# Performance work log

Measured on AMD Instinct MI355X. Metric: run time of the kernel, lower is better.

## Reference

```python
import jax, jax.numpy as jnp
import numpy as np

S, B, N, DIM = 64, 4, 256, 256
HEADS, DIM_HEAD = 8, 32
INNER = HEADS * DIM_HEAD  # 256
SCALE = DIM_HEAD ** -0.5
NEG = -1e10


def setup_inputs() -> dict:
    key = jax.random.key(0)
    k1, k2, k3, k4, k5 = jax.random.split(key, 5)
    x = jax.random.normal(k1, (S, B, N, DIM), dtype=jnp.float32)
    mask = jax.random.randint(k2, (S, N, N), 0, 2, dtype=jnp.int32)
    # nn.Linear(dim, inner*3, bias=False): y = x @ W_qkv  (W stored transposed)
    W_qkv = jax.random.normal(k3, (DIM, 3 * INNER), dtype=jnp.float32) / np.sqrt(DIM)
    W_out = jax.random.normal(k4, (INNER, DIM), dtype=jnp.float32) / np.sqrt(INNER)
    b_out = jax.random.normal(k5, (DIM,), dtype=jnp.float32) * 0.01
    return {"x": x, "mask": mask, "W_qkv": W_qkv, "W_out": W_out, "b_out": b_out}


def reference(x, mask, W_qkv, W_out, b_out):
    s, b, n, _ = x.shape
    qkv = x @ W_qkv                                  # [s,b,n,3*inner]
    q, k, v = jnp.split(qkv, 3, axis=-1)
    def to_heads(t):
        # s b n (h d) -> s b h n d
        return t.reshape(s, b, n, HEADS, DIM_HEAD).transpose(0, 1, 3, 2, 4)
    q, k, v = to_heads(q), to_heads(k), to_heads(v)
    sim = jnp.einsum('sbhid,sbhjd->sbhij', q, k) * SCALE
    sim = jnp.where(mask[:, None, None, :, :] == 0, NEG, sim)
    attn = jax.nn.softmax(sim, axis=-1)
    out = jnp.einsum('sbhij,sbhjd->sbhid', attn, v)
    out = out.transpose(0, 1, 3, 2, 4).reshape(s, b, n, INNER)  # s b h n d -> s b n (h d)
    return out @ W_out + b_out
```

## Files before the change

kernel.cpp:

```cpp
#include <hip/hip_runtime.h>

typedef __attribute__((ext_vector_type(8))) short bf16x8;
typedef __attribute__((ext_vector_type(4))) float f32x4;

__device__ __forceinline__ unsigned short f2bf(float f) {
  unsigned int u = __builtin_bit_cast(unsigned int, f);
  u += 0x7fffu + ((u >> 16) & 1u);
  return (unsigned short)(u >> 16);
}

__device__ __forceinline__ unsigned int cvt_pk_bf16(float lo, float hi) {
  unsigned int r;
  asm("v_cvt_pk_bf16_f32 %0, %1, %2" : "=v"(r) : "v"(lo), "v"(hi));
  return r;
}

typedef const __attribute__((address_space(1))) unsigned int* as1_u32p;
typedef __attribute__((address_space(3))) unsigned int* as3_u32p;
__device__ __forceinline__ void glds16(const void* g, void* l) {
  __builtin_amdgcn_global_load_lds((as1_u32p)g, (as3_u32p)l, 16, 0, 0);
}

__global__ __launch_bounds__(256) void cvt_kernel(const float* __restrict__ X,
                                                  unsigned short* __restrict__ Y) {
  const long long i = ((long long)blockIdx.x * 256 + threadIdx.x) * 8;
  float4 a = *reinterpret_cast<const float4*>(X + i);
  float4 b = *reinterpret_cast<const float4*>(X + i + 4);
  bf16x8 t;
  t[0] = (short)f2bf(a.x); t[1] = (short)f2bf(a.y);
  t[2] = (short)f2bf(a.z); t[3] = (short)f2bf(a.w);
  t[4] = (short)f2bf(b.x); t[5] = (short)f2bf(b.y);
  t[6] = (short)f2bf(b.z); t[7] = (short)f2bf(b.w);
  *reinterpret_cast<bf16x8*>(Y + i) = t;
}

__global__ __launch_bounds__(256) void transpose_bf16_kernel(
    const float* __restrict__ S, unsigned short* __restrict__ D, int R, int C) {
  __shared__ float T[32][33];
  const int bx = blockIdx.x * 32;
  const int by = blockIdx.y * 32;
  const int tx = threadIdx.x & 31, ty = threadIdx.x >> 5;
#pragma unroll
  for (int k = 0; k < 4; ++k)
    T[ty + 8 * k][tx] = S[(size_t)(by + ty + 8 * k) * C + bx + tx];
  __syncthreads();
#pragma unroll
  for (int k = 0; k < 4; ++k)
    D[(size_t)(bx + ty + 8 * k) * R + by + tx] = f2bf(T[tx][ty + 8 * k]);
}

__global__ __launch_bounds__(256) void pack_mask_kernel(const int* __restrict__ mask,
                                                        unsigned int* __restrict__ Mb) {
  const int g = blockIdx.x * 256 + threadIdx.x;
  const unsigned long long bal = __ballot(mask[g] != 0);
  const int lane = threadIdx.x & 63;
  if ((lane & 31) == 0)
    Mb[g >> 5] = (unsigned int)(bal >> (lane & 32));
}

template <bool C_F32>
__global__ __launch_bounds__(256) void gemm_bt(
    const unsigned short* __restrict__ A,
    const unsigned short* __restrict__ Bt,
    void* __restrict__ Cv,
    const float* __restrict__ bias,
    int M, int N, int K)
{
  __shared__ __align__(16) unsigned short As[2][128 * 32];
  __shared__ __align__(16) unsigned short Bs[2][128 * 32];

  const int tid  = threadIdx.x;
  const int bm   = blockIdx.x * 128;
  const int bn   = blockIdx.y * 128;
  const int lane = tid & 63;
  const int wave = tid >> 6;
  const int wr   = (wave >> 1) * 64;
  const int wc   = (wave & 1) * 64;
  const int l15  = lane & 15;
  const int quad = lane >> 4;

  f32x4 acc[4][4];
#pragma unroll
  for (int r = 0; r < 4; ++r)
#pragma unroll
    for (int c = 0; c < 4; ++c) {
      f32x4 z = {0.f, 0.f, 0.f, 0.f};
      acc[r][c] = z;
    }

  const unsigned short* gA0 = A  + (size_t)(bm + wave * 16 + (lane >> 2)) * K + (lane & 3) * 8;
  const unsigned short* gA1 = gA0 + (size_t)64 * K;
  const unsigned short* gB0 = Bt + (size_t)(bn + wave * 16 + (lane >> 2)) * K + (lane & 3) * 8;
  const unsigned short* gB1 = gB0 + (size_t)64 * K;
  const int woff = wave * 512;

  glds16(gA0, &As[0][woff]);
  glds16(gA1, &As[0][2048 + woff]);
  glds16(gB0, &Bs[0][woff]);
  glds16(gB1, &Bs[0][2048 + woff]);
  __syncthreads();

  const int nt = K >> 5;
  for (int t = 0; t < nt; ++t) {
    const int cur = t & 1;
    if (t + 1 < nt) {
      const int kk = (t + 1) << 5;
      unsigned short* an = As[cur ^ 1];
      unsigned short* bn_ = Bs[cur ^ 1];
      glds16(gA0 + kk, an + woff);
      glds16(gA1 + kk, an + 2048 + woff);
      glds16(gB0 + kk, bn_ + woff);
      glds16(gB1 + kk, bn_ + 2048 + woff);
    }
    bf16x8 af[4], bf[4];
#pragma unroll
    for (int i = 0; i < 4; ++i) {
      af[i] = *reinterpret_cast<const bf16x8*>(&As[cur][(wr + i * 16 + l15) * 32 + quad * 8]);
      bf[i] = *reinterpret_cast<const bf16x8*>(&Bs[cur][(wc + i * 16 + l15) * 32 + quad * 8]);
    }
#pragma unroll
    for (int rt = 0; rt < 4; ++rt)
#pragma unroll
      for (int ct = 0; ct < 4; ++ct)
        acc[rt][ct] = __builtin_amdgcn_mfma_f32_16x16x32_bf16(af[rt], bf[ct], acc[rt][ct], 0, 0, 0);
    __syncthreads();
  }

#pragma unroll
  for (int rt = 0; rt < 4; ++rt)
#pragma unroll
    for (int ct = 0; ct < 4; ++ct)
#pragma unroll
      for (int i = 0; i < 4; ++i) {
        const int row = bm + wr + rt * 16 + quad * 4 + i;
        const int col = bn + wc + ct * 16 + l15;
        const float v = acc[rt][ct][i];
        if constexpr (C_F32) {
          ((float*)Cv)[(size_t)row * N + col] = v + bias[col];
        } else {
          ((unsigned short*)Cv)[(size_t)row * N + col] = f2bf(v);
        }
      }
}

#define SCALE_F 0.17677669529663689f

__global__ __launch_bounds__(256) void attn_kernel(
    const unsigned short* __restrict__ QKV,
    const unsigned int* __restrict__ Mb,
    unsigned short* __restrict__ Aout)
{
  __shared__ __align__(16) unsigned short Ks[256 * 32];
  __shared__ __align__(16) unsigned short Vs[256 * 36];

  const int blk  = blockIdx.x;
  const int h    = blk & 7;
  const int sb   = blk >> 3;
  const int s    = sb >> 2;
  const int t0   = sb << 8;
  const int tid  = threadIdx.x;
  const int lane = tid & 63;
  const int wave = tid >> 6;
  const int l15  = lane & 15;
  const int quad = lane >> 4;

  {
    const unsigned short* kp = QKV + (size_t)(t0 + tid) * 768 + 256 + h * 32;
    const unsigned short* vp = kp + 256;
    const int sw = (tid >> 1) & 3;
    unsigned short* kd = Ks + tid * 32;
    unsigned short* vd = Vs + tid * 36;
#pragma unroll
    for (int g = 0; g < 4; ++g)
      *reinterpret_cast<uint4*>(kd + ((g ^ sw) << 3)) = *reinterpret_cast<const uint4*>(kp + g * 8);
#pragma unroll
    for (int i = 0; i < 16; ++i)
      *reinterpret_cast<unsigned int*>(vd + i * 2) = *reinterpret_cast<const unsigned int*>(vp + i * 2);
  }
  __syncthreads();

  bf16x8 bv[2][8];
#pragma unroll
  for (int dt = 0; dt < 2; ++dt)
#pragma unroll
    for (int c = 0; c < 8; ++c) {
      bf16x8 v;
#pragma unroll
      for (int j = 0; j < 8; ++j) {
        const int row = c * 32 + ((j < 4) ? (quad * 4 + j) : (16 + quad * 4 + (j - 4)));
        v[j] = (short)Vs[row * 36 + dt * 16 + l15];
      }
      bv[dt][c] = v;
    }

  const int swr = (l15 >> 1) & 3;

  for (int qb = 0; qb < 4; ++qb) {
    const int qbase = wave * 64 + qb * 16;

    bf16x8 qf = *reinterpret_cast<const bf16x8*>(
        QKV + (size_t)(t0 + qbase + l15) * 768 + h * 32 + quad * 8);

    unsigned int msk[8];
    {
      const unsigned int* mrow = Mb + (((size_t)s * 256 + qbase + l15) << 3);
      uint4 m0 = *reinterpret_cast<const uint4*>(mrow);
      uint4 m1 = *reinterpret_cast<const uint4*>(mrow + 4);
      const int qs = quad * 4;
      msk[0] = m0.x >> qs; msk[1] = m0.y >> qs; msk[2] = m0.z >> qs; msk[3] = m0.w >> qs;
      msk[4] = m1.x >> qs; msk[5] = m1.y >> qs; msk[6] = m1.z >> qs; msk[7] = m1.w >> qs;
    }

    f32x4 sim[16];
#pragma unroll
    for (int ct = 0; ct < 16; ++ct) {
      bf16x8 kf = *reinterpret_cast<const bf16x8*>(
          &Ks[(ct * 16 + l15) * 32 + ((quad ^ swr) << 3)]);
      f32x4 z = {0.f, 0.f, 0.f, 0.f};
      sim[ct] = __builtin_amdgcn_mfma_f32_16x16x32_bf16(kf, qf, z, 0, 0, 0);
    }

    float mx = -3.0e38f;
#pragma unroll
    for (int ct = 0; ct < 16; ++ct)
#pragma unroll
      for (int i = 0; i < 4; ++i) {
        float v = sim[ct][i] * SCALE_F;
        if (!((msk[ct >> 1] >> ((ct & 1) * 16 + i)) & 1u)) v = -1.0e10f;
        sim[ct][i] = v;
        mx = fmaxf(mx, v);
      }
    mx = fmaxf(mx, __shfl_xor(mx, 16, 64));
    mx = fmaxf(mx, __shfl_xor(mx, 32, 64));

    float sum = 0.f;
#pragma unroll
    for (int ct = 0; ct < 16; ++ct)
#pragma unroll
      for (int i = 0; i < 4; ++i) {
        float e = __expf(sim[ct][i] - mx);
        sim[ct][i] = e;
        sum += e;
      }
    sum += __shfl_xor(sum, 16, 64);
    sum += __shfl_xor(sum, 32, 64);
    const float rl = 1.0f / sum;

    f32x4 o0 = {0.f, 0.f, 0.f, 0.f};
    f32x4 o1 = {0.f, 0.f, 0.f, 0.f};
#pragma unroll
    for (int c = 0; c < 8; ++c) {
      uint4 u;
      u.x = cvt_pk_bf16(sim[2 * c][0] * rl,     sim[2 * c][1] * rl);
      u.y = cvt_pk_bf16(sim[2 * c][2] * rl,     sim[2 * c][3] * rl);
      u.z = cvt_pk_bf16(sim[2 * c + 1][0] * rl, sim[2 * c + 1][1] * rl);
      u.w = cvt_pk_bf16(sim[2 * c + 1][2] * rl, sim[2 * c + 1][3] * rl);
      bf16x8 pf = __builtin_bit_cast(bf16x8, u);
      o0 = __builtin_amdgcn_mfma_f32_16x16x32_bf16(pf, bv[0][c], o0, 0, 0, 0);
      o1 = __builtin_amdgcn_mfma_f32_16x16x32_bf16(pf, bv[1][c], o1, 0, 0, 0);
    }

#pragma unroll
    for (int i = 0; i < 4; ++i) {
      const size_t row = (size_t)t0 + qbase + quad * 4 + i;
      Aout[row * 256 + h * 32 + l15]      = f2bf(o0[i]);
      Aout[row * 256 + h * 32 + 16 + l15] = f2bf(o1[i]);
    }
  }
}

extern "C" void kernel_launch(void* const* d_in, const int* in_sizes, int n_in,
                              void* d_out, int out_size, void* d_ws, size_t ws_size,
                              hipStream_t stream) {
  const float* X    = (const float*)d_in[0];
  const int*   mask = (const int*)d_in[1];
  const float* Wqkv = (const float*)d_in[2];
  const float* Wout = (const float*)d_in[3];
  const float* bout = (const float*)d_in[4];
  float*       outp = (float*)d_out;

  unsigned short* QKV   = (unsigned short*)d_ws;
  unsigned short* Xbf   = QKV + (size_t)65536 * 768;
  unsigned short* Amid  = Xbf;
  unsigned short* WoutT = QKV;
  unsigned short* WqkvT = (unsigned short*)d_out;
  unsigned int*   Mbits = (unsigned int*)((char*)d_out + ((size_t)32 << 20));

  dim3 blk(256);
  cvt_kernel<<<dim3(8192), blk, 0, stream>>>(X, Xbf);
  transpose_bf16_kernel<<<dim3(24, 8), blk, 0, stream>>>(Wqkv, WqkvT, 256, 768);
  pack_mask_kernel<<<dim3(16384), blk, 0, stream>>>(mask, Mbits);

  gemm_bt<false><<<dim3(512, 6), blk, 0, stream>>>(Xbf, WqkvT, (void*)QKV, nullptr, 65536, 768, 256);
  attn_kernel<<<dim3(2048), blk, 0, stream>>>(QKV, Mbits, Amid);

  transpose_bf16_kernel<<<dim3(8, 8), blk, 0, stream>>>(Wout, WoutT, 256, 256);
  gemm_bt<true><<<dim3(512, 2), blk, 0, stream>>>(Amid, WoutT, (void*)outp, bout, 65536, 256, 256);
}
```

Baseline: 311.4 us.

## Single-buffer GEMM LDS, transpose V in LDS, defer softmax normalization

The GEMM drops LDS double buffering for a single buffer loaded and synced each k-step. The attention kernel gets a launch-bounds occupancy hint and preloads all Q fragments. It stores V transposed in LDS and reads it per MFMA instead of holding it in registers. Masking becomes a bitmask AND after exp, and the 1/sum normalization moves onto the output. These cut register pressure to raise occupancy, at the cost of losing load/compute overlap in the GEMM. A fully masked row now gives a zero sum where it used to give a uniform distribution.

Measured after the change: 338.0 us. 1.09x slower.

```diff
diff --git a/kernel.cpp b/kernel.cpp
--- a/kernel.cpp
+++ b/kernel.cpp
@@ -66,8 +66,8 @@
     const float* __restrict__ bias,
     int M, int N, int K)
 {
-  __shared__ __align__(16) unsigned short As[2][128 * 32];
-  __shared__ __align__(16) unsigned short Bs[2][128 * 32];
+  __shared__ __align__(16) unsigned short As[128 * 32];
+  __shared__ __align__(16) unsigned short Bs[128 * 32];
 
   const int tid  = threadIdx.x;
   const int bm   = blockIdx.x * 128;
@@ -92,31 +92,23 @@
   const unsigned short* gA1 = gA0 + (size_t)64 * K;
   const unsigned short* gB0 = Bt + (size_t)(bn + wave * 16 + (lane >> 2)) * K + (lane & 3) * 8;
   const unsigned short* gB1 = gB0 + (size_t)64 * K;
-  const int woff = wave * 512;
-
-  glds16(gA0, &As[0][woff]);
-  glds16(gA1, &As[0][2048 + woff]);
-  glds16(gB0, &Bs[0][woff]);
-  glds16(gB1, &Bs[0][2048 + woff]);
-  __syncthreads();
-
-  const int nt = K >> 5;
-  for (int t = 0; t < nt; ++t) {
-    const int cur = t & 1;
-    if (t + 1 < nt) {
-      const int kk = (t + 1) << 5;
-      unsigned short* an = As[cur ^ 1];
-      unsigned short* bn_ = Bs[cur ^ 1];
-      glds16(gA0 + kk, an + woff);
-      glds16(gA1 + kk, an + 2048 + woff);
-      glds16(gB0 + kk, bn_ + woff);
-      glds16(gB1 + kk, bn_ + 2048 + woff);
-    }
+  unsigned short* lA0 = As + wave * 512;
+  unsigned short* lA1 = As + 2048 + wave * 512;
+  unsigned short* lB0 = Bs + wave * 512;
+  unsigned short* lB1 = Bs + 2048 + wave * 512;
+
+  for (int kk = 0; kk < K; kk += 32) {
+    glds16(gA0 + kk, lA0);
+    glds16(gA1 + kk, lA1);
+    glds16(gB0 + kk, lB0);
+    glds16(gB1 + kk, lB1);
+    __syncthreads();
+
     bf16x8 af[4], bf[4];
 #pragma unroll
     for (int i = 0; i < 4; ++i) {
-      af[i] = *reinterpret_cast<const bf16x8*>(&As[cur][(wr + i * 16 + l15) * 32 + quad * 8]);
-      bf[i] = *reinterpret_cast<const bf16x8*>(&Bs[cur][(wc + i * 16 + l15) * 32 + quad * 8]);
+      af[i] = *reinterpret_cast<const bf16x8*>(&As[(wr + i * 16 + l15) * 32 + quad * 8]);
+      bf[i] = *reinterpret_cast<const bf16x8*>(&Bs[(wc + i * 16 + l15) * 32 + quad * 8]);
     }
 #pragma unroll
     for (int rt = 0; rt < 4; ++rt)
@@ -145,13 +137,13 @@
 
 #define SCALE_F 0.17677669529663689f
 
-__global__ __launch_bounds__(256) void attn_kernel(
+__global__ __launch_bounds__(256, 4) void attn_kernel(
     const unsigned short* __restrict__ QKV,
     const unsigned int* __restrict__ Mb,
     unsigned short* __restrict__ Aout)
 {
   __shared__ __align__(16) unsigned short Ks[256 * 32];
-  __shared__ __align__(16) unsigned short Vs[256 * 36];
+  __shared__ __align__(16) unsigned short Vt[32 * 264];
 
   const int blk  = blockIdx.x;
   const int h    = blk & 7;
@@ -164,51 +156,49 @@
   const int l15  = lane & 15;
   const int quad = lane >> 4;
 
+  bf16x8 qf[4];
+#pragma unroll
+  for (int qb = 0; qb < 4; ++qb)
+    qf[qb] = *reinterpret_cast<const bf16x8*>(
+        QKV + (size_t)(t0 + wave * 64 + qb * 16 + l15) * 768 + h * 32 + quad * 8);
+
   {
     const unsigned short* kp = QKV + (size_t)(t0 + tid) * 768 + 256 + h * 32;
     const unsigned short* vp = kp + 256;
     const int sw = (tid >> 1) & 3;
     unsigned short* kd = Ks + tid * 32;
-    unsigned short* vd = Vs + tid * 36;
 #pragma unroll
     for (int g = 0; g < 4; ++g)
       *reinterpret_cast<uint4*>(kd + ((g ^ sw) << 3)) = *reinterpret_cast<const uint4*>(kp + g * 8);
-#pragma unroll
-    for (int i = 0; i < 16; ++i)
-      *reinterpret_cast<unsigned int*>(vd + i * 2) = *reinterpret_cast<const unsigned int*>(vp + i * 2);
+    uint4 v0 = *reinterpret_cast<const uint4*>(vp);
+    uint4 v1 = *reinterpret_cast<const uint4*>(vp + 8);
+    uint4 v2 = *reinterpret_cast<const uint4*>(vp + 16);
+    uint4 v3 = *reinterpret_cast<const uint4*>(vp + 24);
+    unsigned int dw[16] = {v0.x, v0.y, v0.z, v0.w, v1.x, v1.y, v1.z, v1.w,
+                           v2.x, v2.y, v2.z, v2.w, v3.x, v3.y, v3.z, v3.w};
+#pragma unroll
+    for (int w = 0; w < 16; ++w) {
+      Vt[(2 * w) * 264 + tid]     = (unsigned short)dw[w];
+      Vt[(2 * w + 1) * 264 + tid] = (unsigned short)(dw[w] >> 16);
+    }
   }
   __syncthreads();
 
-  bf16x8 bv[2][8];
-#pragma unroll
-  for (int dt = 0; dt < 2; ++dt)
-#pragma unroll
-    for (int c = 0; c < 8; ++c) {
-      bf16x8 v;
-#pragma unroll
-      for (int j = 0; j < 8; ++j) {
-        const int row = c * 32 + ((j < 4) ? (quad * 4 + j) : (16 + quad * 4 + (j - 4)));
-        v[j] = (short)Vs[row * 36 + dt * 16 + l15];
-      }
-      bv[dt][c] = v;
-    }
-
   const int swr = (l15 >> 1) & 3;
+  const int q4  = quad * 4;
+  const unsigned short* vr0 = Vt + l15 * 264;
+  const unsigned short* vr1 = Vt + (16 + l15) * 264;
 
   for (int qb = 0; qb < 4; ++qb) {
     const int qbase = wave * 64 + qb * 16;
-
-    bf16x8 qf = *reinterpret_cast<const bf16x8*>(
-        QKV + (size_t)(t0 + qbase + l15) * 768 + h * 32 + quad * 8);
 
     unsigned int msk[8];
     {
       const unsigned int* mrow = Mb + (((size_t)s * 256 + qbase + l15) << 3);
       uint4 m0 = *reinterpret_cast<const uint4*>(mrow);
       uint4 m1 = *reinterpret_cast<const uint4*>(mrow + 4);
-      const int qs = quad * 4;
-      msk[0] = m0.x >> qs; msk[1] = m0.y >> qs; msk[2] = m0.z >> qs; msk[3] = m0.w >> qs;
-      msk[4] = m1.x >> qs; msk[5] = m1.y >> qs; msk[6] = m1.z >> qs; msk[7] = m1.w >> qs;
+      msk[0] = m0.x >> q4; msk[1] = m0.y >> q4; msk[2] = m0.z >> q4; msk[3] = m0.w >> q4;
+      msk[4] = m1.x >> q4; msk[5] = m1.y >> q4; msk[6] = m1.z >> q4; msk[7] = m1.w >> q4;
     }
 
     f32x4 sim[16];
@@ -217,54 +207,63 @@
       bf16x8 kf = *reinterpret_cast<const bf16x8*>(
           &Ks[(ct * 16 + l15) * 32 + ((quad ^ swr) << 3)]);
       f32x4 z = {0.f, 0.f, 0.f, 0.f};
-      sim[ct] = __builtin_amdgcn_mfma_f32_16x16x32_bf16(kf, qf, z, 0, 0, 0);
+      sim[ct] = __builtin_amdgcn_mfma_f32_16x16x32_bf16(kf, qf[qb], z, 0, 0, 0);
     }
 
     float mx = -3.0e38f;
 #pragma unroll
     for (int ct = 0; ct < 16; ++ct)
 #pragma unroll
-      for (int i = 0; i < 4; ++i) {
-        float v = sim[ct][i] * SCALE_F;
-        if (!((msk[ct >> 1] >> ((ct & 1) * 16 + i)) & 1u)) v = -1.0e10f;
-        sim[ct][i] = v;
-        mx = fmaxf(mx, v);
-      }
+      for (int i = 0; i < 4; ++i)
+        mx = fmaxf(mx, sim[ct][i]);
     mx = fmaxf(mx, __shfl_xor(mx, 16, 64));
     mx = fmaxf(mx, __shfl_xor(mx, 32, 64));
+    const float nms = -mx * SCALE_F;
 
     float sum = 0.f;
 #pragma unroll
     for (int ct = 0; ct < 16; ++ct)
 #pragma unroll
       for (int i = 0; i < 4; ++i) {
-        float e = __expf(sim[ct][i] - mx);
+        float e = __expf(fmaf(sim[ct][i], SCALE_F, nms));
+        const int keep = __builtin_amdgcn_sbfe((int)msk[ct >> 1], (ct & 1) * 16 + i, 1);
+        e = __builtin_bit_cast(float, __builtin_bit_cast(int, e) & keep);
         sim[ct][i] = e;
         sum += e;
       }
     sum += __shfl_xor(sum, 16, 64);
     sum += __shfl_xor(sum, 32, 64);
-    const float rl = 1.0f / sum;
+
+    float rl[4];
+#pragma unroll
+    for (int i = 0; i < 4; ++i)
+      rl[i] = 1.0f / __shfl(sum, q4 + i, 64);
 
     f32x4 o0 = {0.f, 0.f, 0.f, 0.f};
     f32x4 o1 = {0.f, 0.f, 0.f, 0.f};
 #pragma unroll
     for (int c = 0; c < 8; ++c) {
       uint4 u;
-      u.x = cvt_pk_bf16(sim[2 * c][0] * rl,     sim[2 * c][1] * rl);
-      u.y = cvt_pk_bf16(sim[2 * c][2] * rl,     sim[2 * c][3] * rl);
-      u.z = cvt_pk_bf16(sim[2 * c + 1][0] * rl, sim[2 * c + 1][1] * rl);
-      u.w = cvt_pk_bf16(sim[2 * c + 1][2] * rl, sim[2 * c + 1][3] * rl);
+      u.x = cvt_pk_bf16(sim[2 * c][0],     sim[2 * c][1]);
+      u.y = cvt_pk_bf16(sim[2 * c][2],     sim[2 * c][3]);
+      u.z = cvt_pk_bf16(sim[2 * c + 1][0], sim[2 * c + 1][1]);
+      u.w = cvt_pk_bf16(sim[2 * c + 1][2], sim[2 * c + 1][3]);
       bf16x8 pf = __builtin_bit_cast(bf16x8, u);
-      o0 = __builtin_amdgcn_mfma_f32_16x16x32_bf16(pf, bv[0][c], o0, 0, 0, 0);
-      o1 = __builtin_amdgcn_mfma_f32_16x16x32_bf16(pf, bv[1][c], o1, 0, 0, 0);
+      uint2 a0 = *reinterpret_cast<const uint2*>(vr0 + c * 32 + q4);
+      uint2 b0 = *reinterpret_cast<const uint2*>(vr0 + c * 32 + 16 + q4);
+      uint2 a1 = *reinterpret_cast<const uint2*>(vr1 + c * 32 + q4);
+      uint2 b1 = *reinterpret_cast<const uint2*>(vr1 + c * 32 + 16 + q4);
+      uint4 u0v = {a0.x, a0.y, b0.x, b0.y};
+      uint4 u1v = {a1.x, a1.y, b1.x, b1.y};
+      o0 = __builtin_amdgcn_mfma_f32_16x16x32_bf16(pf, __builtin_bit_cast(bf16x8, u0v), o0, 0, 0, 0);
+      o1 = __builtin_amdgcn_mfma_f32_16x16x32_bf16(pf, __builtin_bit_cast(bf16x8, u1v), o1, 0, 0, 0);
     }
 
 #pragma unroll
     for (int i = 0; i < 4; ++i) {
       const size_t row = (size_t)t0 + qbase + quad * 4 + i;
-      Aout[row * 256 + h * 32 + l15]      = f2bf(o0[i]);
-      Aout[row * 256 + h * 32 + 16 + l15] = f2bf(o1[i]);
+      Aout[row * 256 + h * 32 + l15]      = f2bf(o0[i] * rl[i]);
+      Aout[row * 256 + h * 32 + 16 + l15] = f2bf(o1[i] * rl[i]);
     }
   }
 }
```
